# Kernel tuning notes

Measured on AMD Instinct MI355X. Metric: run time of the kernel, lower is better.

Reference implementation:

```python
import jax, jax.numpy as jnp
import numpy as np

N, D, H, E = 32768, 2048, 4096, 8  # tokens, d_model, hidden_size, num_experts


def setup_inputs() -> dict:
    key = jax.random.key(0)
    k1, k2, k3 = jax.random.split(key, 3)
    x = jax.random.normal(k1, (N, D), dtype=jnp.float32)
    w_up_gate = jax.random.normal(k2, (E, 2 * H, D), dtype=jnp.float32) * (D ** -0.5)
    w_down = jax.random.normal(k3, (E, H, D), dtype=jnp.float32) * (H ** -0.5)
    # equal token counts per expert (grouped-GEMM batch sizes)
    batch_size_per_expert = jnp.full((E,), N // E, dtype=jnp.int32)
    return {"x": x, "w_up_gate": w_up_gate, "w_down": w_down,
            "batch_size_per_expert": batch_size_per_expert}


def reference(x, w_up_gate, w_down, batch_size_per_expert):
    # Grouped GEMM with equal group sizes == batched GEMM over experts.
    e, two_h, d = w_up_gate.shape
    h_dim = two_h // 2
    xt = x.reshape(e, -1, d)                      # [E, T, D], T tokens per expert
    # gmm(x, w_up_gate, trans_b=True): per-expert x @ w_up_gate[e].T
    up_gate = jnp.einsum('etd,ehd->eth', xt, w_up_gate)  # [E, T, 2H]
    up, gate = up_gate[..., :h_dim], up_gate[..., h_dim:]
    hidden = up * jax.nn.silu(gate)               # fused SwiGLU
    # gmm(h, w_down, trans_b=False): per-expert h @ w_down[e]
    down = jnp.einsum('eth,ehd->etd', hidden, w_down)    # [E, T, D]
    return down.reshape(-1, d)
```

## Files before the change

kernel.cpp:

```cpp
#include <hip/hip_runtime.h>
#include <hip/hip_bf16.h>
#include <cstdint>
#include <cstddef>

#define NTOK 32768
#define DDIM 2048
#define HDIM 4096
#define NEXP 8
#define TTOK 4096

typedef __attribute__((ext_vector_type(8))) __bf16 bf16x8;
typedef __attribute__((ext_vector_type(4))) float f32x4;

#define MFMA_BF16(a, b, c) __builtin_amdgcn_mfma_f32_16x16x32_bf16((a), (b), (c), 0, 0, 0)
#define SBAR() __builtin_amdgcn_s_barrier()
#define SCHED0() __builtin_amdgcn_sched_barrier(0)
#define WAIT_VM(n) asm volatile("s_waitcnt vmcnt(" #n ")" ::: "memory")
#define WAIT_LGKM0() asm volatile("s_waitcnt lgkmcnt(0)" ::: "memory")

__device__ __forceinline__ unsigned short f2bf(float f) {
  unsigned int u = __builtin_bit_cast(unsigned int, f);
  u += 0x7FFFu + ((u >> 16) & 1u);
  return (unsigned short)(u >> 16);
}

__global__ __launch_bounds__(256) void cvt_kernel(const float* __restrict__ src,
                                                  unsigned short* __restrict__ dst,
                                                  long n4) {
  long i = (long)blockIdx.x * blockDim.x + threadIdx.x;
  long stride = (long)gridDim.x * blockDim.x;
  const float4* s4 = (const float4*)src;
  ushort4* d4 = (ushort4*)dst;
  for (; i < n4; i += stride) {
    float4 v = s4[i];
    ushort4 o;
    o.x = f2bf(v.x); o.y = f2bf(v.y); o.z = f2bf(v.z); o.w = f2bf(v.w);
    d4[i] = o;
  }
}

__global__ __launch_bounds__(256) void transpose_wd(const float* __restrict__ w,
                                                    unsigned short* __restrict__ wt) {
  __shared__ unsigned short tile[64][66];
  const int e = blockIdx.z;
  const int h0 = blockIdx.y * 64;
  const int d0 = blockIdx.x * 64;
  const float* we = w + (size_t)e * HDIM * DDIM;
  unsigned short* wte = wt + (size_t)e * DDIM * HDIM;
  const int t = threadIdx.x;
  const int r = t >> 4;
  const int c4 = (t & 15) * 4;
#pragma unroll
  for (int p = 0; p < 4; ++p) {
    int h = r + p * 16;
    float4 v = *(const float4*)(we + (size_t)(h0 + h) * DDIM + d0 + c4);
    tile[h][c4 + 0] = f2bf(v.x);
    tile[h][c4 + 1] = f2bf(v.y);
    tile[h][c4 + 2] = f2bf(v.z);
    tile[h][c4 + 3] = f2bf(v.w);
  }
  __syncthreads();
#pragma unroll
  for (int p = 0; p < 4; ++p) {
    int d = r + p * 16;
    ushort4 o;
    o.x = tile[c4 + 0][d];
    o.y = tile[c4 + 1][d];
    o.z = tile[c4 + 2][d];
    o.w = tile[c4 + 3][d];
    *(ushort4*)(wte + (size_t)(d0 + d) * HDIM + h0 + c4) = o;
  }
}

__device__ __forceinline__ void stage128x64(const unsigned short* __restrict__ g0,
                                            size_t stride_elems,
                                            unsigned short* lds, int tid) {
#pragma unroll
  for (int i = 0; i < 4; ++i) {
    int gi = i * 256 + tid;
    int r = gi >> 3;
    int c = gi & 7;
    const unsigned short* src = g0 + (size_t)r * stride_elems + ((c ^ (r & 7)) << 3);
    __builtin_amdgcn_global_load_lds(
        (const __attribute__((address_space(1))) unsigned int*)src,
        (__attribute__((address_space(3))) unsigned int*)(lds + (size_t)gi * 8),
        16, 0, 0);
  }
}

__device__ __forceinline__ bf16x8 read_frag(const unsigned short* lds, int row, int cg) {
  return *(const bf16x8*)(lds + row * 64 + ((cg ^ (row & 7)) << 3));
}

__global__ __launch_bounds__(256, 2) void gemm1_swiglu(
    const unsigned short* __restrict__ Xb,
    const unsigned short* __restrict__ Wb,
    unsigned short* __restrict__ Hid) {
  __shared__ unsigned short sA[128 * 64];
  __shared__ unsigned short sBu[2][128 * 64];
  __shared__ unsigned short sBg[2][128 * 64];
  const int bn = blockIdx.x;
  const int bm = blockIdx.y;
  const int e  = blockIdx.z;
  const unsigned short* Xe = Xb + ((size_t)e * TTOK + bm * 128) * DDIM;
  const unsigned short* Wu = Wb + ((size_t)e * 2 * HDIM + (size_t)bn * 128) * DDIM;
  const unsigned short* Wg = Wu + (size_t)HDIM * DDIM;
  const int tid = threadIdx.x;
  const int lane = tid & 63;
  const int wid = tid >> 6;
  const int wm = (wid & 1) * 64;
  const int wn = (wid >> 1) * 64;
  const int lr = lane & 15;
  const int lk = lane >> 4;

  f32x4 au[4][4], ag[4][4];
#pragma unroll
  for (int i = 0; i < 4; ++i)
#pragma unroll
    for (int j = 0; j < 4; ++j) {
      au[i][j] = f32x4{0.f, 0.f, 0.f, 0.f};
      ag[i][j] = f32x4{0.f, 0.f, 0.f, 0.f};
    }

  const int NT = DDIM / 64;
  stage128x64(Wu, DDIM, sBu[0], tid);
  stage128x64(Wg, DDIM, sBg[0], tid);
  stage128x64(Xe, DDIM, sA, tid);
  stage128x64(Wu + 64, DDIM, sBu[1], tid);
  stage128x64(Wg + 64, DDIM, sBg[1], tid);

  for (int t = 0; t < NT; ++t) {
    const int cur = t & 1;
    if (t + 1 < NT) { WAIT_VM(8); } else { WAIT_VM(0); }
    SBAR();
    SCHED0();
    const unsigned short* bu = sBu[cur];
    const unsigned short* bg = sBg[cur];
#pragma unroll
    for (int kh = 0; kh < 2; ++kh) {
      const int cg = kh * 4 + lk;
      bf16x8 a[4], u[4], g[4];
#pragma unroll
      for (int mi = 0; mi < 4; ++mi) a[mi] = read_frag(sA, wm + mi * 16 + lr, cg);
#pragma unroll
      for (int ni = 0; ni < 4; ++ni) u[ni] = read_frag(bu, wn + ni * 16 + lr, cg);
#pragma unroll
      for (int ni = 0; ni < 4; ++ni) g[ni] = read_frag(bg, wn + ni * 16 + lr, cg);
#pragma unroll
      for (int mi = 0; mi < 4; ++mi)
#pragma unroll
        for (int ni = 0; ni < 4; ++ni) {
          au[mi][ni] = MFMA_BF16(a[mi], u[ni], au[mi][ni]);
          ag[mi][ni] = MFMA_BF16(a[mi], g[ni], ag[mi][ni]);
        }
    }
    SCHED0();
    WAIT_LGKM0();
    SBAR();
    SCHED0();
    if (t + 1 < NT) stage128x64(Xe + (t + 1) * 64, DDIM, sA, tid);
    if (t + 2 < NT) {
      stage128x64(Wu + (t + 2) * 64, DDIM, sBu[cur], tid);
      stage128x64(Wg + (t + 2) * 64, DDIM, sBg[cur], tid);
    }
  }

  unsigned short* He = Hid + ((size_t)e * TTOK + bm * 128) * HDIM + (size_t)bn * 128;
#pragma unroll
  for (int mi = 0; mi < 4; ++mi)
#pragma unroll
    for (int ni = 0; ni < 4; ++ni)
#pragma unroll
      for (int r = 0; r < 4; ++r) {
        int row = wm + mi * 16 + lk * 4 + r;
        int col = wn + ni * 16 + lr;
        float up = au[mi][ni][r];
        float gv = ag[mi][ni][r];
        He[(size_t)row * HDIM + col] = f2bf(up * gv / (1.f + __expf(-gv)));
      }
}

__global__ __launch_bounds__(256, 2) void gemm2_down(
    const unsigned short* __restrict__ Hid,
    const unsigned short* __restrict__ WdT,
    float* __restrict__ Out) {
  __shared__ unsigned short sA[2][128 * 64];
  __shared__ unsigned short sB[2][128 * 64];
  const int bn = blockIdx.x;
  const int bm = blockIdx.y;
  const int e  = blockIdx.z;
  const unsigned short* Ae = Hid + ((size_t)e * TTOK + bm * 128) * HDIM;
  const unsigned short* Be = WdT + ((size_t)e * DDIM + (size_t)bn * 128) * HDIM;
  const int tid = threadIdx.x;
  const int lane = tid & 63;
  const int wid = tid >> 6;
  const int wm = (wid & 1) * 64;
  const int wn = (wid >> 1) * 64;
  const int lr = lane & 15;
  const int lk = lane >> 4;

  f32x4 acc[4][4];
#pragma unroll
  for (int i = 0; i < 4; ++i)
#pragma unroll
    for (int j = 0; j < 4; ++j) acc[i][j] = f32x4{0.f, 0.f, 0.f, 0.f};

  const int NT = HDIM / 64;
  stage128x64(Ae, HDIM, sA[0], tid);
  stage128x64(Be, HDIM, sB[0], tid);
  stage128x64(Ae + 64, HDIM, sA[1], tid);
  stage128x64(Be + 64, HDIM, sB[1], tid);

  for (int t = 0; t < NT; ++t) {
    const int cur = t & 1;
    if (t + 1 < NT) { WAIT_VM(8); } else { WAIT_VM(0); }
    SBAR();
    SCHED0();
    const unsigned short* a = sA[cur];
    const unsigned short* b = sB[cur];
#pragma unroll
    for (int kh = 0; kh < 2; ++kh) {
      const int cg = kh * 4 + lk;
      bf16x8 af[4], bf[4];
#pragma unroll
      for (int mi = 0; mi < 4; ++mi) af[mi] = read_frag(a, wm + mi * 16 + lr, cg);
#pragma unroll
      for (int ni = 0; ni < 4; ++ni) bf[ni] = read_frag(b, wn + ni * 16 + lr, cg);
#pragma unroll
      for (int mi = 0; mi < 4; ++mi)
#pragma unroll
        for (int ni = 0; ni < 4; ++ni)
          acc[mi][ni] = MFMA_BF16(af[mi], bf[ni], acc[mi][ni]);
    }
    SCHED0();
    WAIT_LGKM0();
    SBAR();
    SCHED0();
    if (t + 2 < NT) {
      stage128x64(Ae + (t + 2) * 64, HDIM, sA[cur], tid);
      stage128x64(Be + (t + 2) * 64, HDIM, sB[cur], tid);
    }
  }

  float* Oe = Out + ((size_t)e * TTOK + bm * 128) * DDIM + (size_t)bn * 128;
#pragma unroll
  for (int mi = 0; mi < 4; ++mi)
#pragma unroll
    for (int ni = 0; ni < 4; ++ni)
#pragma unroll
      for (int r = 0; r < 4; ++r) {
        int row = wm + mi * 16 + lk * 4 + r;
        int col = wn + ni * 16 + lr;
        Oe[(size_t)row * DDIM + col] = acc[mi][ni][r];
      }
}

extern "C" void kernel_launch(void* const* d_in, const int* in_sizes, int n_in,
                              void* d_out, int out_size, void* d_ws, size_t ws_size,
                              hipStream_t stream) {
  const float* x = (const float*)d_in[0];
  const float* wug = (const float*)d_in[1];
  const float* wd = (const float*)d_in[2];
  float* out = (float*)d_out;

  unsigned short* xb   = (unsigned short*)d_ws;
  unsigned short* wugb = xb   + (size_t)NTOK * DDIM;
  unsigned short* wdT  = wugb + (size_t)NEXP * 2 * HDIM * DDIM;
  unsigned short* hid  = wdT  + (size_t)NEXP * DDIM * HDIM;

  cvt_kernel<<<4096, 256, 0, stream>>>(x, xb, (long)NTOK * DDIM / 4);
  cvt_kernel<<<4096, 256, 0, stream>>>(wug, wugb, (long)NEXP * 2 * HDIM * DDIM / 4);
  transpose_wd<<<dim3(DDIM / 64, HDIM / 64, NEXP), 256, 0, stream>>>(wd, wdT);
  gemm1_swiglu<<<dim3(HDIM / 128, TTOK / 128, NEXP), 256, 0, stream>>>(xb, wugb, hid);
  gemm2_down<<<dim3(DDIM / 128, TTOK / 128, NEXP), 256, 0, stream>>>(hid, wdT, out);
}
```

Baseline: 1.948 ms.

## Load A fragments directly from global into registers, shrink GEMM1 N tile

Both GEMMs stop staging the activation tile in LDS. Each wave now loads its A fragments straight from global memory into registers, one k-step ahead, while B is still double-buffered through LDS. GEMM1's N tile drops from 128 to 64 so it can use one combined up/gate buffer, and launch bounds go up to 3 blocks per CU. The aim is to cut LDS footprint and LDS read traffic to raise occupancy. In exchange, A reuse across waves is lost: the two waves sharing each row block read the same rows from global/L2, and GEMM1 now runs twice as many blocks, each re-reading X.

```diff
diff --git a/kernel.cpp b/kernel.cpp
--- a/kernel.cpp
+++ b/kernel.cpp
@@ -72,9 +72,25 @@
   }
 }
 
-__device__ __forceinline__ void stage128x64(const unsigned short* __restrict__ g0,
-                                            size_t stride_elems,
-                                            unsigned short* lds, int tid) {
+__device__ __forceinline__ void stage64(const unsigned short* __restrict__ g0,
+                                        size_t stride_elems,
+                                        unsigned short* lds, int tid) {
+#pragma unroll
+  for (int i = 0; i < 2; ++i) {
+    int gi = i * 256 + tid;
+    int r = gi >> 3;
+    int c = gi & 7;
+    const unsigned short* src = g0 + (size_t)r * stride_elems + ((c ^ (r & 7)) << 3);
+    __builtin_amdgcn_global_load_lds(
+        (const __attribute__((address_space(1))) unsigned int*)src,
+        (__attribute__((address_space(3))) unsigned int*)(lds + (size_t)gi * 8),
+        16, 0, 0);
+  }
+}
+
+__device__ __forceinline__ void stage128(const unsigned short* __restrict__ g0,
+                                         size_t stride_elems,
+                                         unsigned short* lds, int tid) {
 #pragma unroll
   for (int i = 0; i < 4; ++i) {
     int gi = i * 256 + tid;
@@ -92,84 +108,94 @@
   return *(const bf16x8*)(lds + row * 64 + ((cg ^ (row & 7)) << 3));
 }
 
-__global__ __launch_bounds__(256, 2) void gemm1_swiglu(
+__global__ __launch_bounds__(256, 3) void gemm1_swiglu(
     const unsigned short* __restrict__ Xb,
     const unsigned short* __restrict__ Wb,
     unsigned short* __restrict__ Hid) {
-  __shared__ unsigned short sA[128 * 64];
-  __shared__ unsigned short sBu[2][128 * 64];
-  __shared__ unsigned short sBg[2][128 * 64];
+  __shared__ unsigned short sB[2][128 * 64];
   const int bn = blockIdx.x;
   const int bm = blockIdx.y;
   const int e  = blockIdx.z;
   const unsigned short* Xe = Xb + ((size_t)e * TTOK + bm * 128) * DDIM;
-  const unsigned short* Wu = Wb + ((size_t)e * 2 * HDIM + (size_t)bn * 128) * DDIM;
+  const unsigned short* Wu = Wb + ((size_t)e * 2 * HDIM + (size_t)bn * 64) * DDIM;
   const unsigned short* Wg = Wu + (size_t)HDIM * DDIM;
   const int tid = threadIdx.x;
   const int lane = tid & 63;
   const int wid = tid >> 6;
   const int wm = (wid & 1) * 64;
-  const int wn = (wid >> 1) * 64;
+  const int wn = (wid >> 1) * 32;
   const int lr = lane & 15;
   const int lk = lane >> 4;
 
-  f32x4 au[4][4], ag[4][4];
+  const unsigned short* ap = Xe + (size_t)(wm + lr) * DDIM + lk * 8;
+
+  f32x4 au[4][2], ag[4][2];
 #pragma unroll
   for (int i = 0; i < 4; ++i)
 #pragma unroll
-    for (int j = 0; j < 4; ++j) {
+    for (int j = 0; j < 2; ++j) {
       au[i][j] = f32x4{0.f, 0.f, 0.f, 0.f};
       ag[i][j] = f32x4{0.f, 0.f, 0.f, 0.f};
     }
 
+  auto stageB = [&](int t) {
+    stage64(Wu + t * 64, DDIM, (unsigned short*)sB[t & 1], tid);
+    stage64(Wg + t * 64, DDIM, (unsigned short*)sB[t & 1] + 64 * 64, tid);
+  };
+
+  bf16x8 a[4][2];
   const int NT = DDIM / 64;
-  stage128x64(Wu, DDIM, sBu[0], tid);
-  stage128x64(Wg, DDIM, sBg[0], tid);
-  stage128x64(Xe, DDIM, sA, tid);
-  stage128x64(Wu + 64, DDIM, sBu[1], tid);
-  stage128x64(Wg + 64, DDIM, sBg[1], tid);
+  stageB(0);
+  SCHED0();
+#pragma unroll
+  for (int mi = 0; mi < 4; ++mi)
+#pragma unroll
+    for (int kh = 0; kh < 2; ++kh)
+      a[mi][kh] = *(const bf16x8*)(ap + (size_t)mi * 16 * DDIM + kh * 32);
+  SCHED0();
+  stageB(1);
 
   for (int t = 0; t < NT; ++t) {
-    const int cur = t & 1;
-    if (t + 1 < NT) { WAIT_VM(8); } else { WAIT_VM(0); }
+    if (t + 1 < NT) { WAIT_VM(4); } else { WAIT_VM(0); }
     SBAR();
     SCHED0();
-    const unsigned short* bu = sBu[cur];
-    const unsigned short* bg = sBg[cur];
+    const unsigned short* B = sB[t & 1];
 #pragma unroll
     for (int kh = 0; kh < 2; ++kh) {
       const int cg = kh * 4 + lk;
-      bf16x8 a[4], u[4], g[4];
-#pragma unroll
-      for (int mi = 0; mi < 4; ++mi) a[mi] = read_frag(sA, wm + mi * 16 + lr, cg);
-#pragma unroll
-      for (int ni = 0; ni < 4; ++ni) u[ni] = read_frag(bu, wn + ni * 16 + lr, cg);
-#pragma unroll
-      for (int ni = 0; ni < 4; ++ni) g[ni] = read_frag(bg, wn + ni * 16 + lr, cg);
-#pragma unroll
-      for (int mi = 0; mi < 4; ++mi)
-#pragma unroll
-        for (int ni = 0; ni < 4; ++ni) {
-          au[mi][ni] = MFMA_BF16(a[mi], u[ni], au[mi][ni]);
-          ag[mi][ni] = MFMA_BF16(a[mi], g[ni], ag[mi][ni]);
-        }
+      bf16x8 u0 = read_frag(B, wn + lr, cg);
+      bf16x8 u1 = read_frag(B, wn + 16 + lr, cg);
+      bf16x8 g0 = read_frag(B, 64 + wn + lr, cg);
+      bf16x8 g1 = read_frag(B, 64 + wn + 16 + lr, cg);
+#pragma unroll
+      for (int mi = 0; mi < 4; ++mi) {
+        au[mi][0] = MFMA_BF16(a[mi][kh], u0, au[mi][0]);
+        au[mi][1] = MFMA_BF16(a[mi][kh], u1, au[mi][1]);
+        ag[mi][0] = MFMA_BF16(a[mi][kh], g0, ag[mi][0]);
+        ag[mi][1] = MFMA_BF16(a[mi][kh], g1, ag[mi][1]);
+      }
     }
     SCHED0();
     WAIT_LGKM0();
     SBAR();
     SCHED0();
-    if (t + 1 < NT) stage128x64(Xe + (t + 1) * 64, DDIM, sA, tid);
-    if (t + 2 < NT) {
-      stage128x64(Wu + (t + 2) * 64, DDIM, sBu[cur], tid);
-      stage128x64(Wg + (t + 2) * 64, DDIM, sBg[cur], tid);
-    }
-  }
-
-  unsigned short* He = Hid + ((size_t)e * TTOK + bm * 128) * HDIM + (size_t)bn * 128;
+    if (t + 1 < NT) {
+#pragma unroll
+      for (int mi = 0; mi < 4; ++mi)
+#pragma unroll
+        for (int kh = 0; kh < 2; ++kh)
+          a[mi][kh] = *(const bf16x8*)(ap + (size_t)mi * 16 * DDIM + (t + 1) * 64 + kh * 32);
+    }
+    SCHED0();
+    if (t + 2 < NT) stageB(t + 2);
+    SCHED0();
+  }
+
+  unsigned short* He = Hid + ((size_t)e * TTOK + bm * 128) * HDIM + (size_t)bn * 64;
 #pragma unroll
   for (int mi = 0; mi < 4; ++mi)
 #pragma unroll
-    for (int ni = 0; ni < 4; ++ni)
+    for (int ni = 0; ni < 2; ++ni)
 #pragma unroll
       for (int r = 0; r < 4; ++r) {
         int row = wm + mi * 16 + lk * 4 + r;
@@ -180,11 +206,10 @@
       }
 }
 
-__global__ __launch_bounds__(256, 2) void gemm2_down(
+__global__ __launch_bounds__(256, 3) void gemm2_down(
     const unsigned short* __restrict__ Hid,
     const unsigned short* __restrict__ WdT,
     float* __restrict__ Out) {
-  __shared__ unsigned short sA[2][128 * 64];
   __shared__ unsigned short sB[2][128 * 64];
   const int bn = blockIdx.x;
   const int bm = blockIdx.y;
@@ -199,47 +224,64 @@
   const int lr = lane & 15;
   const int lk = lane >> 4;
 
+  const unsigned short* ap = Ae + (size_t)(wm + lr) * HDIM + lk * 8;
+
   f32x4 acc[4][4];
 #pragma unroll
   for (int i = 0; i < 4; ++i)
 #pragma unroll
     for (int j = 0; j < 4; ++j) acc[i][j] = f32x4{0.f, 0.f, 0.f, 0.f};
 
+  auto stageB = [&](int t) {
+    stage128(Be + t * 64, HDIM, (unsigned short*)sB[t & 1], tid);
+  };
+
+  bf16x8 a[4][2];
   const int NT = HDIM / 64;
-  stage128x64(Ae, HDIM, sA[0], tid);
-  stage128x64(Be, HDIM, sB[0], tid);
-  stage128x64(Ae + 64, HDIM, sA[1], tid);
-  stage128x64(Be + 64, HDIM, sB[1], tid);
+  stageB(0);
+  SCHED0();
+#pragma unroll
+  for (int mi = 0; mi < 4; ++mi)
+#pragma unroll
+    for (int kh = 0; kh < 2; ++kh)
+      a[mi][kh] = *(const bf16x8*)(ap + (size_t)mi * 16 * HDIM + kh * 32);
+  SCHED0();
+  stageB(1);
 
   for (int t = 0; t < NT; ++t) {
-    const int cur = t & 1;
-    if (t + 1 < NT) { WAIT_VM(8); } else { WAIT_VM(0); }
+    if (t + 1 < NT) { WAIT_VM(4); } else { WAIT_VM(0); }
     SBAR();
     SCHED0();
-    const unsigned short* a = sA[cur];
-    const unsigned short* b = sB[cur];
+    const unsigned short* B = sB[t & 1];
 #pragma unroll
     for (int kh = 0; kh < 2; ++kh) {
       const int cg = kh * 4 + lk;
-      bf16x8 af[4], bf[4];
-#pragma unroll
-      for (int mi = 0; mi < 4; ++mi) af[mi] = read_frag(a, wm + mi * 16 + lr, cg);
-#pragma unroll
-      for (int ni = 0; ni < 4; ++ni) bf[ni] = read_frag(b, wn + ni * 16 + lr, cg);
-#pragma unroll
-      for (int mi = 0; mi < 4; ++mi)
-#pragma unroll
-        for (int ni = 0; ni < 4; ++ni)
-          acc[mi][ni] = MFMA_BF16(af[mi], bf[ni], acc[mi][ni]);
+      bf16x8 b0 = read_frag(B, wn + lr, cg);
+      bf16x8 b1 = read_frag(B, wn + 16 + lr, cg);
+      bf16x8 b2 = read_frag(B, wn + 32 + lr, cg);
+      bf16x8 b3 = read_frag(B, wn + 48 + lr, cg);
+#pragma unroll
+      for (int mi = 0; mi < 4; ++mi) {
+        acc[mi][0] = MFMA_BF16(a[mi][kh], b0, acc[mi][0]);
+        acc[mi][1] = MFMA_BF16(a[mi][kh], b1, acc[mi][1]);
+        acc[mi][2] = MFMA_BF16(a[mi][kh], b2, acc[mi][2]);
+        acc[mi][3] = MFMA_BF16(a[mi][kh], b3, acc[mi][3]);
+      }
     }
     SCHED0();
     WAIT_LGKM0();
     SBAR();
     SCHED0();
-    if (t + 2 < NT) {
-      stage128x64(Ae + (t + 2) * 64, HDIM, sA[cur], tid);
-      stage128x64(Be + (t + 2) * 64, HDIM, sB[cur], tid);
-    }
+    if (t + 1 < NT) {
+#pragma unroll
+      for (int mi = 0; mi < 4; ++mi)
+#pragma unroll
+        for (int kh = 0; kh < 2; ++kh)
+          a[mi][kh] = *(const bf16x8*)(ap + (size_t)mi * 16 * HDIM + (t + 1) * 64 + kh * 32);
+    }
+    SCHED0();
+    if (t + 2 < NT) stageB(t + 2);
+    SCHED0();
   }
 
   float* Oe = Out + ((size_t)e * TTOK + bm * 128) * DDIM + (size_t)bn * 128;
@@ -271,6 +313,6 @@
   cvt_kernel<<<4096, 256, 0, stream>>>(x, xb, (long)NTOK * DDIM / 4);
   cvt_kernel<<<4096, 256, 0, stream>>>(wug, wugb, (long)NEXP * 2 * HDIM * DDIM / 4);
   transpose_wd<<<dim3(DDIM / 64, HDIM / 64, NEXP), 256, 0, stream>>>(wd, wdT);
-  gemm1_swiglu<<<dim3(HDIM / 128, TTOK / 128, NEXP), 256, 0, stream>>>(xb, wugb, hid);
+  gemm1_swiglu<<<dim3(HDIM / 64, TTOK / 128, NEXP), 256, 0, stream>>>(xb, wugb, hid);
   gemm2_down<<<dim3(DDIM / 128, TTOK / 128, NEXP), 256, 0, stream>>>(hid, wdT, out);
 }
```

New measurement: 3.446 ms. +76.9%, slower.
